# Kernel tuning notes

Measured on AMD Instinct MI355X. Metric: run time of the kernel, lower is better.

The kernel has to match this reference:

```python
import math
import jax, jax.numpy as jnp
import numpy as np

HEAD_DIM = 2
ROPE_PERIOD = 19.0
OMEGA = 2.0 * math.pi / ROPE_PERIOD
PEAK_EPS = 0.3
TARGET_LOGIT_GAP = math.log(10.0)
ATTN_AMPLITUDE = TARGET_LOGIT_GAP / (math.cos(OMEGA * PEAK_EPS) - math.cos(OMEGA * (1.0 - PEAK_EPS)))
QK_NORM_SCALE = math.sqrt(ATTN_AMPLITUDE / math.sqrt(2.0))
SCALE = HEAD_DIM ** (-0.5) * QK_NORM_SCALE ** 2
INTERMEDIATE_SIZE = 2
EMBED_CONST = 1000.0
B, L = 4, 4096


def _rms(x, eps=1e-6):
    return x * jax.lax.rsqrt(jnp.mean(x * x, axis=-1, keepdims=True) + eps)


def _rope(x):
    # x: (B, 1, L, 2)
    seq_len = x.shape[2]
    theta = jnp.arange(seq_len, dtype=x.dtype) * jnp.asarray(OMEGA, x.dtype)
    cos_t = jnp.cos(theta)[None, None, :, None]
    sin_t = jnp.sin(theta)[None, None, :, None]
    x0, x1 = x[..., 0:1], x[..., 1:2]
    return jnp.concatenate([x0 * cos_t - x1 * sin_t, x0 * sin_t + x1 * cos_t], axis=-1)


def setup_inputs() -> dict:
    key = jax.random.key(0)
    k1, k2, k3, k4, k5 = jax.random.split(key, 5)
    x = jax.random.normal(k1, (B, L, 2), dtype=jnp.float32)
    # causal additive mask (1, 1, L, L)
    causal = jnp.tril(jnp.ones((L, L), dtype=bool))
    mask = jnp.where(causal, 0.0, -1e9).astype(jnp.float32)[None, None]
    q_weight = jax.random.normal(k2, (1,), dtype=jnp.float32) * 0.1
    v_weight = jax.random.normal(k3, (1,), dtype=jnp.float32) * 0.1
    gate_weight = jax.random.normal(k4, (2,), dtype=jnp.float32) * 0.1
    carry_weight = jax.random.normal(k5, (1,), dtype=jnp.float32) * 0.1
    return {"x": x, "mask": mask, "q_weight": q_weight, "v_weight": v_weight,
            "gate_weight": gate_weight, "carry_weight": carry_weight}


def reference(x, mask, q_weight, v_weight, gate_weight, carry_weight):
    # ---- attention branch ----
    xn = _rms(x)                                    # (B, L, 2)
    phi = q_weight[0]
    q = jnp.stack([xn[..., 0] * jnp.cos(phi), xn[..., 0] * -jnp.sin(phi)], axis=-1)
    k = jnp.stack([xn[..., 0], jnp.zeros_like(xn[..., 0])], axis=-1)
    v = jnp.stack([xn[..., 1] * v_weight[0], jnp.zeros_like(xn[..., 0])], axis=-1)
    q, k, v = q[:, None], k[:, None], v[:, None]    # (B, 1, L, 2)
    q = _rope(_rms(q))
    k = _rope(_rms(k))
    attn = jnp.einsum('bhqd,bhkd->bhqk', q, k) * jnp.asarray(SCALE, x.dtype)
    attn = jax.nn.softmax(attn + mask, axis=-1)
    out = jnp.einsum('bhqk,bhkd->bhqd', attn, v)    # (B, 1, L, 2)
    o0 = out[:, 0, :, 0]                            # (B, L)
    attn_out = jnp.stack([jnp.zeros_like(o0), o0], axis=-1)  # OProj channel swap
    h = x + attn_out
    # ---- gated MLP branch ----
    hn = _rms(h)
    a, c = gate_weight[0], gate_weight[1]
    g0 = hn[..., 0] * a + hn[..., 1] * c
    g1 = hn[..., 0] * (a - c / EMBED_CONST) + hn[..., 1] * c
    base = hn[..., 0]
    mix0 = jax.nn.silu(g0) * base
    mix1 = jax.nn.silu(g1) * base
    y1 = carry_weight[0] * (mix1 - mix0)
    mlp_out = jnp.stack([jnp.zeros_like(y1), y1], axis=-1)
    return h + mlp_out
```

## Files before the change

kernel.cpp:

```cpp
#include <hip/hip_runtime.h>
#include <math.h>

#define SEQ_L 4096
#define THREADS 512
#define WAVES 8
#define BLOCKS_PER_BATCH 256

__global__ __launch_bounds__(THREADS) void attn_rows_kernel(
    const float* __restrict__ x,
    const float* __restrict__ q_weight,
    const float* __restrict__ v_weight,
    const float* __restrict__ gate_weight,
    const float* __restrict__ carry_weight,
    float* __restrict__ out,
    float scaleL2,
    float omega,
    float cd, float sd,
    float ck1, float sk1,
    float ck2, float sk2,
    float ck3, float sk3)
{
    __shared__ float As[SEQ_L];
    __shared__ float Ws[SEQ_L];

    const int tid  = threadIdx.x;
    const int lane = tid & 63;
    const int wave = tid >> 6;
    const int b    = blockIdx.x >> 8;
    const int bb   = blockIdx.x & 255;

    const float phi = q_weight[0];
    const float vw  = v_weight[0];
    const float2* x2 = (const float2*)x + (size_t)b * SEQ_L;

    for (int j = tid; j < SEQ_L; j += THREADS) {
        float2 xv = x2[j];
        float inv = rsqrtf((xv.x * xv.x + xv.y * xv.y) * 0.5f + 1e-6f);
        float xn0 = xv.x * inv;
        float xn1 = xv.y * inv;
        As[j] = xn0 * rsqrtf(xn0 * xn0 * 0.5f + 1e-6f);
        Ws[j] = xn1 * vw;
    }
    __syncthreads();

    const float ga = gate_weight[0];
    const float gc = gate_weight[1];
    const float cw = carry_weight[0];

    const int v = bb * WAVES + wave;
    const float SQRT2 = 1.4142135623730951f;
    const float LOG2E = 1.4426950408889634f;

    #pragma unroll
    for (int rr = 0; rr < 2; ++rr) {
        const int i = (rr == 0) ? v : (SEQ_L - 1 - v);

        const float t2 = scaleL2 * As[i];
        const float M2 = fabsf(t2) * SQRT2;

        unsigned r = (unsigned)(i - (lane << 2) + 266) % 19u;
        float th = omega * (float)r - phi;
        float C = t2 * cosf(th);
        float S = t2 * sinf(th);

        float ssum = 0.f, osum = 0.f;
        int jb = lane << 2;
        const int nfull = (i + 1) >> 8;

        for (int k = 0; k < nfull; ++k) {
            float4 av = *(const float4*)&As[jb];
            float4 wv = *(const float4*)&Ws[jb];
            float C1 = fmaf(S, sk1, C * ck1);
            float C2 = fmaf(S, sk2, C * ck2);
            float C3 = fmaf(S, sk3, C * ck3);
            float e0 = __builtin_amdgcn_exp2f(fmaf(av.x, C,  -M2));
            float e1 = __builtin_amdgcn_exp2f(fmaf(av.y, C1, -M2));
            float e2 = __builtin_amdgcn_exp2f(fmaf(av.z, C2, -M2));
            float e3 = __builtin_amdgcn_exp2f(fmaf(av.w, C3, -M2));
            ssum += (e0 + e1) + (e2 + e3);
            osum = fmaf(e0, wv.x, osum);
            osum = fmaf(e1, wv.y, osum);
            osum = fmaf(e2, wv.z, osum);
            osum = fmaf(e3, wv.w, osum);
            float Cn = fmaf(S, sd, C * cd);
            float Sn = fmaf(S, cd, -(C * sd));
            C = Cn; S = Sn;
            jb += 256;
        }
        {
            float4 av = *(const float4*)&As[jb];
            float4 wv = *(const float4*)&Ws[jb];
            float C1 = fmaf(S, sk1, C * ck1);
            float C2 = fmaf(S, sk2, C * ck2);
            float C3 = fmaf(S, sk3, C * ck3);
            float e0 = __builtin_amdgcn_exp2f(fmaf(av.x, C,  -M2));
            float e1 = __builtin_amdgcn_exp2f(fmaf(av.y, C1, -M2));
            float e2 = __builtin_amdgcn_exp2f(fmaf(av.z, C2, -M2));
            float e3 = __builtin_amdgcn_exp2f(fmaf(av.w, C3, -M2));
            e0 = (jb + 0 <= i) ? e0 : 0.f;
            e1 = (jb + 1 <= i) ? e1 : 0.f;
            e2 = (jb + 2 <= i) ? e2 : 0.f;
            e3 = (jb + 3 <= i) ? e3 : 0.f;
            ssum += (e0 + e1) + (e2 + e3);
            osum = fmaf(e0, wv.x, osum);
            osum = fmaf(e1, wv.y, osum);
            osum = fmaf(e2, wv.z, osum);
            osum = fmaf(e3, wv.w, osum);
        }

        for (int off = 32; off > 0; off >>= 1) {
            ssum += __shfl_xor(ssum, off);
            osum += __shfl_xor(osum, off);
        }

        if (lane == 0) {
            float o0 = osum * __builtin_amdgcn_rcpf(ssum);
            float2 xv = x2[i];
            float h0 = xv.x;
            float h1 = xv.y + o0;
            float inv = __builtin_amdgcn_rsqf(
                           fmaf(h0, h0 * 0.5f, fmaf(h1, h1 * 0.5f, 1e-6f)));
            float hn0 = h0 * inv, hn1 = h1 * inv;
            float g0 = hn0 * ga + hn1 * gc;
            float g1 = hn0 * (ga - gc * 1e-3f) + hn1 * gc;
            float sig0 = __builtin_amdgcn_rcpf(1.f + __builtin_amdgcn_exp2f(-g0 * LOG2E));
            float sig1 = __builtin_amdgcn_rcpf(1.f + __builtin_amdgcn_exp2f(-g1 * LOG2E));
            float mix0 = g0 * sig0 * hn0;
            float mix1 = g1 * sig1 * hn0;
            float y1 = cw * (mix1 - mix0);
            float2* outp = (float2*)out + (size_t)b * SEQ_L + i;
            *outp = make_float2(xv.x, h1 + y1);
        }
    }
}

extern "C" void kernel_launch(void* const* d_in, const int* in_sizes, int n_in,
                              void* d_out, int out_size, void* d_ws, size_t ws_size,
                              hipStream_t stream)
{
    const float* x  = (const float*)d_in[0];
    const float* qw = (const float*)d_in[2];
    const float* vw = (const float*)d_in[3];
    const float* gw = (const float*)d_in[4];
    const float* cw = (const float*)d_in[5];
    float* out = (float*)d_out;

    const double omega = 2.0 * M_PI / 19.0;
    const double amp   = log(10.0) / (cos(omega * 0.3) - cos(omega * 0.7));
    const double qkns2 = amp / sqrt(2.0);
    const double scale = pow(2.0, -0.5) * qkns2;
    const double L2E   = 1.4426950408889634074;
    const double delta = 256.0 * omega;

    attn_rows_kernel<<<dim3(4 * BLOCKS_PER_BATCH), dim3(THREADS), 0, stream>>>(
        x, qw, vw, gw, cw, out,
        (float)(scale * L2E), (float)omega,
        (float)cos(delta),       (float)sin(delta),
        (float)cos(omega),       (float)sin(omega),
        (float)cos(2.0 * omega), (float)sin(2.0 * omega),
        (float)cos(3.0 * omega), (float)sin(3.0 * omega));
}
```

Measured before the change: 18.54 us.

## Pack keys and values as half2 in shared memory and use hardware trig

Keys and values are stored together as one half2 array in shared memory, which halves LDS footprint and cuts the inner loop to a single 128-bit load per step. Per-row setup replaces cosf/sinf with hardware sin/cos on a precomputed phi rotation, and the query's normalised value is recomputed from global x. The inner loop now keeps split accumulators for more instruction-level parallelism, the tail block is skipped when it is empty, and launch bounds request higher occupancy. Rounding keys to fp16 before the exponent, which is scaled by a large factor, risks accuracy loss.

```diff
diff --git a/kernel.cpp b/kernel.cpp
--- a/kernel.cpp
+++ b/kernel.cpp
@@ -1,4 +1,5 @@
 #include <hip/hip_runtime.h>
+#include <hip/hip_fp16.h>
 #include <math.h>
 
 #define SEQ_L 4096
@@ -6,7 +7,7 @@
 #define WAVES 8
 #define BLOCKS_PER_BATCH 256
 
-__global__ __launch_bounds__(THREADS) void attn_rows_kernel(
+__global__ __launch_bounds__(THREADS, 8) void attn_rows_kernel(
     const float* __restrict__ x,
     const float* __restrict__ q_weight,
     const float* __restrict__ v_weight,
@@ -14,14 +15,12 @@
     const float* __restrict__ carry_weight,
     float* __restrict__ out,
     float scaleL2,
-    float omega,
     float cd, float sd,
     float ck1, float sk1,
     float ck2, float sk2,
     float ck3, float sk3)
 {
-    __shared__ float As[SEQ_L];
-    __shared__ float Ws[SEQ_L];
+    __shared__ __half2 aw[SEQ_L];
 
     const int tid  = threadIdx.x;
     const int lane = tid & 63;
@@ -33,13 +32,19 @@
     const float vw  = v_weight[0];
     const float2* x2 = (const float2*)x + (size_t)b * SEQ_L;
 
+    const float INV2PI = 0.15915494309189535f;
+    const float rphi = phi * INV2PI;
+    const float cphi = __builtin_amdgcn_cosf(rphi);
+    const float sphi = __builtin_amdgcn_sinf(rphi);
+
     for (int j = tid; j < SEQ_L; j += THREADS) {
         float2 xv = x2[j];
-        float inv = rsqrtf((xv.x * xv.x + xv.y * xv.y) * 0.5f + 1e-6f);
+        float inv = __builtin_amdgcn_rsqf(
+                        fmaf(xv.x, xv.x * 0.5f, fmaf(xv.y, xv.y * 0.5f, 1e-6f)));
         float xn0 = xv.x * inv;
         float xn1 = xv.y * inv;
-        As[j] = xn0 * rsqrtf(xn0 * xn0 * 0.5f + 1e-6f);
-        Ws[j] = xn1 * vw;
+        float a = xn0 * __builtin_amdgcn_rsqf(fmaf(xn0, xn0 * 0.5f, 1e-6f));
+        aw[j] = __floats2half2_rn(a, xn1 * vw);
     }
     __syncthreads();
 
@@ -50,64 +55,86 @@
     const int v = bb * WAVES + wave;
     const float SQRT2 = 1.4142135623730951f;
     const float LOG2E = 1.4426950408889634f;
+    const float INV19 = 1.0f / 19.0f;
 
     #pragma unroll
     for (int rr = 0; rr < 2; ++rr) {
         const int i = (rr == 0) ? v : (SEQ_L - 1 - v);
 
-        const float t2 = scaleL2 * As[i];
+        const float2 xv = x2[i];
+        float invx = __builtin_amdgcn_rsqf(
+                        fmaf(xv.x, xv.x * 0.5f, fmaf(xv.y, xv.y * 0.5f, 1e-6f)));
+        float xn0i = xv.x * invx;
+        float a_i  = xn0i * __builtin_amdgcn_rsqf(fmaf(xn0i, xn0i * 0.5f, 1e-6f));
+        const float t2 = scaleL2 * a_i;
         const float M2 = fabsf(t2) * SQRT2;
 
         unsigned r = (unsigned)(i - (lane << 2) + 266) % 19u;
-        float th = omega * (float)r - phi;
-        float C = t2 * cosf(th);
-        float S = t2 * sinf(th);
+        float rev = (float)r * INV19;
+        float cr = __builtin_amdgcn_cosf(rev);
+        float sr = __builtin_amdgcn_sinf(rev);
+        float c0 = fmaf(sr, sphi, cr * cphi);
+        float s0 = fmaf(cr, -sphi, sr * cphi);
+        float C = t2 * c0;
+        float S = t2 * s0;
 
-        float ssum = 0.f, osum = 0.f;
+        float sA = 0.f, sB = 0.f, oA = 0.f, oB = 0.f;
         int jb = lane << 2;
         const int nfull = (i + 1) >> 8;
 
         for (int k = 0; k < nfull; ++k) {
-            float4 av = *(const float4*)&As[jb];
-            float4 wv = *(const float4*)&Ws[jb];
+            float4 raw = *(const float4*)&aw[jb];
+            const __half2* hp = (const __half2*)&raw;
+            float2 p0 = __half22float2(hp[0]);
+            float2 p1 = __half22float2(hp[1]);
+            float2 p2 = __half22float2(hp[2]);
+            float2 p3 = __half22float2(hp[3]);
             float C1 = fmaf(S, sk1, C * ck1);
             float C2 = fmaf(S, sk2, C * ck2);
             float C3 = fmaf(S, sk3, C * ck3);
-            float e0 = __builtin_amdgcn_exp2f(fmaf(av.x, C,  -M2));
-            float e1 = __builtin_amdgcn_exp2f(fmaf(av.y, C1, -M2));
-            float e2 = __builtin_amdgcn_exp2f(fmaf(av.z, C2, -M2));
-            float e3 = __builtin_amdgcn_exp2f(fmaf(av.w, C3, -M2));
-            ssum += (e0 + e1) + (e2 + e3);
-            osum = fmaf(e0, wv.x, osum);
-            osum = fmaf(e1, wv.y, osum);
-            osum = fmaf(e2, wv.z, osum);
-            osum = fmaf(e3, wv.w, osum);
+            float e0 = __builtin_amdgcn_exp2f(fmaf(p0.x, C,  -M2));
+            float e1 = __builtin_amdgcn_exp2f(fmaf(p1.x, C1, -M2));
+            float e2 = __builtin_amdgcn_exp2f(fmaf(p2.x, C2, -M2));
+            float e3 = __builtin_amdgcn_exp2f(fmaf(p3.x, C3, -M2));
+            sA += e0 + e1;
+            sB += e2 + e3;
+            oA = fmaf(e0, p0.y, oA);
+            oB = fmaf(e1, p1.y, oB);
+            oA = fmaf(e2, p2.y, oA);
+            oB = fmaf(e3, p3.y, oB);
             float Cn = fmaf(S, sd, C * cd);
             float Sn = fmaf(S, cd, -(C * sd));
             C = Cn; S = Sn;
             jb += 256;
         }
-        {
-            float4 av = *(const float4*)&As[jb];
-            float4 wv = *(const float4*)&Ws[jb];
+        if ((i & 255) != 255) {
+            float4 raw = *(const float4*)&aw[jb];
+            const __half2* hp = (const __half2*)&raw;
+            float2 p0 = __half22float2(hp[0]);
+            float2 p1 = __half22float2(hp[1]);
+            float2 p2 = __half22float2(hp[2]);
+            float2 p3 = __half22float2(hp[3]);
             float C1 = fmaf(S, sk1, C * ck1);
             float C2 = fmaf(S, sk2, C * ck2);
             float C3 = fmaf(S, sk3, C * ck3);
-            float e0 = __builtin_amdgcn_exp2f(fmaf(av.x, C,  -M2));
-            float e1 = __builtin_amdgcn_exp2f(fmaf(av.y, C1, -M2));
-            float e2 = __builtin_amdgcn_exp2f(fmaf(av.z, C2, -M2));
-            float e3 = __builtin_amdgcn_exp2f(fmaf(av.w, C3, -M2));
+            float e0 = __builtin_amdgcn_exp2f(fmaf(p0.x, C,  -M2));
+            float e1 = __builtin_amdgcn_exp2f(fmaf(p1.x, C1, -M2));
+            float e2 = __builtin_amdgcn_exp2f(fmaf(p2.x, C2, -M2));
+            float e3 = __builtin_amdgcn_exp2f(fmaf(p3.x, C3, -M2));
             e0 = (jb + 0 <= i) ? e0 : 0.f;
             e1 = (jb + 1 <= i) ? e1 : 0.f;
             e2 = (jb + 2 <= i) ? e2 : 0.f;
             e3 = (jb + 3 <= i) ? e3 : 0.f;
-            ssum += (e0 + e1) + (e2 + e3);
-            osum = fmaf(e0, wv.x, osum);
-            osum = fmaf(e1, wv.y, osum);
-            osum = fmaf(e2, wv.z, osum);
-            osum = fmaf(e3, wv.w, osum);
+            sA += e0 + e1;
+            sB += e2 + e3;
+            oA = fmaf(e0, p0.y, oA);
+            oB = fmaf(e1, p1.y, oB);
+            oA = fmaf(e2, p2.y, oA);
+            oB = fmaf(e3, p3.y, oB);
         }
 
+        float ssum = sA + sB;
+        float osum = oA + oB;
         for (int off = 32; off > 0; off >>= 1) {
             ssum += __shfl_xor(ssum, off);
             osum += __shfl_xor(osum, off);
@@ -115,7 +142,6 @@
 
         if (lane == 0) {
             float o0 = osum * __builtin_amdgcn_rcpf(ssum);
-            float2 xv = x2[i];
             float h0 = xv.x;
             float h1 = xv.y + o0;
             float inv = __builtin_amdgcn_rsqf(
@@ -154,7 +180,7 @@
 
     attn_rows_kernel<<<dim3(4 * BLOCKS_PER_BATCH), dim3(THREADS), 0, stream>>>(
         x, qw, vw, gw, cw, out,
-        (float)(scale * L2E), (float)omega,
+        (float)(scale * L2E),
         (float)cos(delta),       (float)sin(delta),
         (float)cos(omega),       (float)sin(omega),
         (float)cos(2.0 * omega), (float)sin(2.0 * omega),
```

Result: slower. 19.22 us (+3.7%).
